# Optimization experiments

Measured on AMD Instinct MI355X. Metric: run time of the kernel, lower is better.

The kernel has to match this reference:

```python
import jax, jax.numpy as jnp
import numpy as np

B, L, C, H, W = 1, 16, 16, 128, 256  # L = T_chunk = K_chunk (single chunk, causal)
DECAY = 0.1  # decay_val


def setup_inputs() -> dict:
    key = jax.random.key(0)
    k1, k2 = jax.random.split(key)
    img = jax.random.normal(k1, (B, L, C, H, W), jnp.float32)
    # flows in normalized [-1,1] grid units; keep displacements modest
    cum_flow = jax.random.normal(k2, (B, L, 2, H, W), jnp.float32) * 0.1
    t = jnp.arange(L)
    mask = (t[:, None] >= t[None, :]).astype(jnp.float32)          # causal [T,K]
    decay_dist = jnp.abs(t[:, None] - t[None, :]).astype(jnp.float32)  # [T,K]
    return {"img": img, "cum_flow": cum_flow, "mask": mask, "decay_dist": decay_dist}


def _bilinear_sample(img, gx, gy):
    # img: [B,K,C,H,W]; gx, gy: [B,K,H,W] in normalized [-1,1] coords.
    # x wraps around (periodic), y clamps -- matching the kernel's index handling.
    ix = (gx + 1.0) * (W * 0.5) - 0.5
    iy = (gy + 1.0) * (H * 0.5) - 0.5
    x0 = jnp.floor(ix)
    y0 = jnp.floor(iy)
    wx = ix - x0  # fractional weights
    wy = iy - y0
    x0i = x0.astype(jnp.int32)
    y0i = y0.astype(jnp.int32)
    x0r = jnp.mod(x0i, W)
    x1r = jnpp = jnp.mod(x0i + 1, W)
    y0c = jnp.clip(y0i, 0, H - 1)
    y1c = jnp.clip(y0i + 1, 0, H - 1)

    K = img.shape[1]
    imgf = img.reshape(B, K, C, H * W)

    def gather(yy, xx):
        idx = (yy * W + xx).reshape(B, K, 1, H * W)  # broadcast over C
        return jnp.take_along_axis(imgf, idx, axis=-1).reshape(B, K, C, H, W)

    va = gather(y0c, x0r)  # (y0, x0)
    vb = gather(y1c, x0r)  # (y1, x0)
    vc = gather(y0c, x1r)  # (y0, x1)
    vd = gather(y1c, x1r)  # (y1, x1)
    wx_ = wx[:, :, None]   # [B,K,1,H,W]
    wy_ = wy[:, :, None]
    return (va * (1.0 - wx_) * (1.0 - wy_) + vb * (1.0 - wx_) * wy_
            + vc * wx_ * (1.0 - wy_) + vd * wx_ * wy_)


def reference(img, cum_flow, mask, decay_dist):
    # base grid (align_corners=False style pixel centers)
    base_x = (jnp.arange(W, dtype=jnp.float32) * (2.0 / W) - 1.0 + 1.0 / W)[None, None, :]  # [1,1,W]
    base_y = (jnp.arange(H, dtype=jnp.float32) * (2.0 / H) - 1.0 + 1.0 / H)[None, :, None]  # [1,H,1]

    weights = mask * jnp.exp(-DECAY * decay_dist)  # [T,K] decay-weighted causal mask
    fx = cum_flow[:, :, 0]  # [B,L,H,W]
    fy = cum_flow[:, :, 1]

    def step(carry, inp):
        ft_x, ft_y, w_row = inp  # ft_*: [B,H,W]; w_row: [K]
        gx = base_x[None] + (ft_x[:, None] - fx)  # [B,K,H,W]
        gy = base_y[None] + (ft_y[:, None] - fy)
        gx = jnp.mod(gx + 1.0, 2.0) - 1.0          # wrap x into [-1,1)
        sampled = _bilinear_sample(img, gx, gy)    # [B,K,C,H,W]
        out_t = jnp.einsum('k,bkchw->bchw', w_row, sampled)
        return carry, out_t

    xs = (jnp.moveaxis(fx, 1, 0), jnp.moveaxis(fy, 1, 0), weights)  # over t
    _, outs = jax.lax.scan(step, 0.0, xs)          # [T,B,C,H,W]
    return jnp.moveaxis(outs, 0, 1)                # [B,T,C,H,W]
```

## Files before the change

### kernel.cpp

```cpp
#include <hip/hip_runtime.h>
#include <hip/hip_fp16.h>

constexpr int Lc = 16;
constexpr int Cc = 16;
constexpr int Hc = 128;
constexpr int Wc = 256;
constexpr float DECAYc = 0.1f;
constexpr int HWc = Hc * Wc;

__global__ __launch_bounds__(256) void transpose_cvt_f16(
    const float* __restrict__ img, __half* __restrict__ imgTh)
{
    const int tid = threadIdx.x;
    const int h2 = tid & 1;
    const int wq = tid >> 1;
    const int kf  = blockIdx.x >> 5;
    const int px0 = (blockIdx.x & 31) * 1024;
    const float* __restrict__ srcb =
        img + (size_t)kf * Cc * HWc + (size_t)(8 * h2) * HWc;
#pragma unroll
    for (int rr = 0; rr < 8; ++rr) {
        const int px = px0 + rr * 128 + wq;
        float v[8];
#pragma unroll
        for (int c = 0; c < 8; ++c) v[c] = srcb[c * HWc + px];
        __half2 h[4];
#pragma unroll
        for (int i = 0; i < 4; ++i)
            h[i] = __float22half2_rn(make_float2(v[2 * i], v[2 * i + 1]));
        *(uint4*)(imgTh + ((size_t)kf * HWc + px) * Cc + 8 * h2) = *(uint4*)h;
    }
}

template <int T0>
__device__ __forceinline__ void chunk8(
    int k, const __half* __restrict__ bkq,
    const float* sx1, const float* sy1, float fxk, float fyk,
    const float* et, float ek, float4* acc)
{
    uint2 ld [8][4];
    float wts[8][4];
    int  offs[8][4];

#pragma unroll
    for (int j = 0; j < 8; ++j) {
        const int t = T0 + j;
        if (t >= Lc) continue;
        if (t > k) {
            const float wkt = et[t] * ek;

            float a = sx1[t] - fxk;
            a -= 2.0f * floorf(a * 0.5f);
            const float X  = a * (Wc * 0.5f) + 255.5f;
            const float Xf = floorf(X);
            const float wx = X - Xf;
            const int xp  = (int)Xf;
            const int x0r = xp & (Wc - 1);
            const int x1r = (xp + 1) & (Wc - 1);

            const float iy = (sy1[t] - fyk) * (Hc * 0.5f) - 0.5f;
            const float Yf = floorf(iy);
            const float wy = iy - Yf;
            const int y0  = (int)Yf;
            const int y0c = min(max(y0, 0), Hc - 1);
            const int y1c = min(max(y0 + 1, 0), Hc - 1);

            const float wb = wkt * wy;
            const float wa = wkt - wb;
            const float omx = 1.0f - wx;
            wts[j][0] = wa * omx;
            wts[j][1] = wa * wx;
            wts[j][2] = wb * omx;
            wts[j][3] = wb * wx;

            const int r0 = y0c << 8, r1 = y1c << 8;
            offs[j][0] = r0 | x0r;
            offs[j][1] = r0 | x1r;
            offs[j][2] = r1 | x0r;
            offs[j][3] = r1 | x1r;
        }
    }
#pragma unroll
    for (int j = 0; j < 8; ++j) {
        const int t = T0 + j;
        if (t >= Lc) continue;
        if (t > k) {
#pragma unroll
            for (int n = 0; n < 4; ++n)
                ld[j][n] = *(const uint2*)(bkq + (size_t)offs[j][n] * Cc);
        }
    }
#pragma unroll
    for (int j = 0; j < 8; ++j) {
        const int t = T0 + j;
        if (t >= Lc) continue;
        if (t > k) {
#pragma unroll
            for (int n = 0; n < 4; ++n) {
                const __half2* hp = (const __half2*)&ld[j][n];
                const float a = wts[j][n];
                acc[t].x += a * __half2float(__low2half (hp[0]));
                acc[t].y += a * __half2float(__high2half(hp[0]));
                acc[t].z += a * __half2float(__low2half (hp[1]));
                acc[t].w += a * __half2float(__high2half(hp[1]));
            }
        }
    }
}

__global__ __launch_bounds__(256, 2) void gridsample_f16(
    const __half* __restrict__ imgTh,
    const float* __restrict__ cum_flow,
    const float* __restrict__ img,
    float* __restrict__ out)
{
    const int tid = threadIdx.x;
    const int q  = tid & 3;
    const int wq = tid >> 2;
    const int b = blockIdx.x;
    const int band = b & 7;
    const int sub  = b >> 3;
    const int h = band * 16 + (sub >> 2);
    const int w = (sub & 3) * 64 + wq;
    const int pix = h * Wc + w;

    const float base_x = w * (2.0f / Wc) - 1.0f + 1.0f / Wc;
    const float base_y = h * (2.0f / Hc) - 1.0f + 1.0f / Hc;

    float sx1[Lc], sy1[Lc], et[Lc];
#pragma unroll
    for (int t = 0; t < Lc; ++t) {
        sx1[t] = base_x + cum_flow[(t * 2 + 0) * HWc + pix] + 1.0f;
        sy1[t] = base_y + cum_flow[(t * 2 + 1) * HWc + pix] + 1.0f;
        et[t]  = __expf(-DECAYc * (float)t);
    }

    float4 acc[Lc];
#pragma unroll
    for (int t = 0; t < Lc; ++t) acc[t] = make_float4(0.f, 0.f, 0.f, 0.f);

    float ek = 1.0f;
    for (int k = 0; k < Lc - 1; ++k) {
        const float fxk = cum_flow[(k * 2 + 0) * HWc + pix];
        const float fyk = cum_flow[(k * 2 + 1) * HWc + pix];
        const __half* __restrict__ bkq =
            imgTh + (size_t)k * HWc * Cc + 4 * q;

        chunk8<1>(k, bkq, sx1, sy1, fxk, fyk, et, ek, acc);
        chunk8<9>(k, bkq, sx1, sy1, fxk, fyk, et, ek, acc);

        ek *= 1.1051709180756477f;
    }

#pragma unroll
    for (int t = 0; t < Lc; ++t) {
        const float* __restrict__ ip = img + ((size_t)t * Cc + 4 * q) * HWc + pix;
        float* __restrict__ op = out + ((size_t)t * Cc + 4 * q) * HWc + pix;
        op[0 * HWc] = acc[t].x + ip[0 * HWc];
        op[1 * HWc] = acc[t].y + ip[1 * HWc];
        op[2 * HWc] = acc[t].z + ip[2 * HWc];
        op[3 * HWc] = acc[t].w + ip[3 * HWc];
    }
}

__global__ __launch_bounds__(256) void gridsample_warp_acc(
    const float* __restrict__ img, const float* __restrict__ cum_flow,
    const float* __restrict__ mask, const float* __restrict__ decay,
    float* __restrict__ out)
{
    const int w = threadIdx.x, h = blockIdx.x, t = blockIdx.y;
    const int pix = h * Wc + w;
    const float base_x = w * (2.0f / Wc) - 1.0f + 1.0f / Wc;
    const float base_y = h * (2.0f / Hc) - 1.0f + 1.0f / Hc;
    const float fxt = cum_flow[(t * 2 + 0) * HWc + pix];
    const float fyt = cum_flow[(t * 2 + 1) * HWc + pix];
    float acc[Cc];
#pragma unroll
    for (int c = 0; c < Cc; ++c) acc[c] = 0.0f;
    for (int k = 0; k <= t; ++k) {
        const float wkt = mask[t * Lc + k] * __expf(-DECAYc * decay[t * Lc + k]);
        const float fxk = cum_flow[(k * 2 + 0) * HWc + pix];
        const float fyk = cum_flow[(k * 2 + 1) * HWc + pix];
        float gx = base_x + (fxt - fxk);
        const float gy = base_y + (fyt - fyk);
        float m = gx + 1.0f;
        m -= 2.0f * floorf(m * 0.5f);
        gx = m - 1.0f;
        const float ix = (gx + 1.0f) * (Wc * 0.5f) - 0.5f;
        const float iy = (gy + 1.0f) * (Hc * 0.5f) - 0.5f;
        const float x0f = floorf(ix), y0f = floorf(iy);
        const float wx = ix - x0f, wy = iy - y0f;
        const int x0 = (int)x0f, y0 = (int)y0f;
        const int x0r = x0 & (Wc - 1), x1r = (x0 + 1) & (Wc - 1);
        const int y0c = min(max(y0, 0), Hc - 1), y1c = min(max(y0 + 1, 0), Hc - 1);
        const float a00 = wkt * (1.0f - wx) * (1.0f - wy);
        const float a01 = wkt * (1.0f - wx) * wy;
        const float a10 = wkt * wx * (1.0f - wy);
        const float a11 = wkt * wx * wy;
        const int o00 = y0c * Wc + x0r, o01 = y1c * Wc + x0r;
        const int o10 = y0c * Wc + x1r, o11 = y1c * Wc + x1r;
        const float* __restrict__ ik = img + (size_t)k * Cc * HWc;
#pragma unroll
        for (int c = 0; c < Cc; ++c) {
            const float* __restrict__ p = ik + c * HWc;
            acc[c] += p[o00] * a00 + p[o01] * a01 + p[o10] * a10 + p[o11] * a11;
        }
    }
    float* __restrict__ op = out + (size_t)t * Cc * HWc + pix;
#pragma unroll
    for (int c = 0; c < Cc; ++c) op[c * HWc] = acc[c];
}

extern "C" void kernel_launch(void* const* d_in, const int* in_sizes, int n_in,
                              void* d_out, int out_size, void* d_ws, size_t ws_size,
                              hipStream_t stream) {
    const float* img      = (const float*)d_in[0];
    const float* cum_flow = (const float*)d_in[1];
    const float* mask     = (const float*)d_in[2];
    const float* decay    = (const float*)d_in[3];
    float* out = (float*)d_out;

    const size_t needed = (size_t)Lc * HWc * Cc * sizeof(__half);
    if (ws_size >= needed) {
        __half* imgTh = (__half*)d_ws;
        transpose_cvt_f16<<<dim3(512), 256, 0, stream>>>(img, imgTh);
        gridsample_f16<<<dim3(512), 256, 0, stream>>>(imgTh, cum_flow, img, out);
    } else {
        dim3 grid(Hc, Lc, 1);
        gridsample_warp_acc<<<grid, Wc, 0, stream>>>(img, cum_flow, mask, decay, out);
    }
}
```

Before: 153.6 us.

## Fuse fp16 transpose into gridsample kernel with atomic grid barrier

Merges the fp16 channel-last transpose kernel into the grid-sample kernel. Every block first converts its slice of the image, then all blocks wait at a global spin barrier built from an atomic counter before sampling. This removes one kernel launch and the gap between kernels, but adds a memset launch and a spin barrier that only works if all 512 blocks are resident at once. The barrier has a guard-count timeout, so if blocks are not co-resident it falls through and could read imgTh before it is written.

```diff
diff --git a/kernel.cpp b/kernel.cpp
--- a/kernel.cpp
+++ b/kernel.cpp
@@ -7,30 +7,7 @@
 constexpr int Wc = 256;
 constexpr float DECAYc = 0.1f;
 constexpr int HWc = Hc * Wc;
-
-__global__ __launch_bounds__(256) void transpose_cvt_f16(
-    const float* __restrict__ img, __half* __restrict__ imgTh)
-{
-    const int tid = threadIdx.x;
-    const int h2 = tid & 1;
-    const int wq = tid >> 1;
-    const int kf  = blockIdx.x >> 5;
-    const int px0 = (blockIdx.x & 31) * 1024;
-    const float* __restrict__ srcb =
-        img + (size_t)kf * Cc * HWc + (size_t)(8 * h2) * HWc;
-#pragma unroll
-    for (int rr = 0; rr < 8; ++rr) {
-        const int px = px0 + rr * 128 + wq;
-        float v[8];
-#pragma unroll
-        for (int c = 0; c < 8; ++c) v[c] = srcb[c * HWc + px];
-        __half2 h[4];
-#pragma unroll
-        for (int i = 0; i < 4; ++i)
-            h[i] = __float22half2_rn(make_float2(v[2 * i], v[2 * i + 1]));
-        *(uint4*)(imgTh + ((size_t)kf * HWc + px) * Cc + 8 * h2) = *(uint4*)h;
-    }
-}
+constexpr unsigned NBLK = 512;
 
 template <int T0>
 __device__ __forceinline__ void chunk8(
@@ -108,16 +85,51 @@
     }
 }
 
-__global__ __launch_bounds__(256, 2) void gridsample_f16(
-    const __half* __restrict__ imgTh,
+__global__ __launch_bounds__(256, 2) void gridsample_fused2(
+    const float* __restrict__ img,
     const float* __restrict__ cum_flow,
-    const float* __restrict__ img,
+    __half* __restrict__ imgTh,
+    unsigned int* __restrict__ done,
     float* __restrict__ out)
 {
     const int tid = threadIdx.x;
+    const int b = blockIdx.x;
+
+    {
+        const int h2 = tid & 1;
+        const int wqa = tid >> 1;
+        const int kf  = b >> 5;
+        const int px0 = (b & 31) * 1024;
+        const float* __restrict__ srcb =
+            img + (size_t)kf * Cc * HWc + (size_t)(8 * h2) * HWc;
+#pragma unroll
+        for (int rr = 0; rr < 8; ++rr) {
+            const int px = px0 + rr * 128 + wqa;
+            float v[8];
+#pragma unroll
+            for (int c = 0; c < 8; ++c) v[c] = srcb[c * HWc + px];
+            __half2 hh[4];
+#pragma unroll
+            for (int i = 0; i < 4; ++i)
+                hh[i] = __float22half2_rn(make_float2(v[2 * i], v[2 * i + 1]));
+            *(uint4*)(imgTh + ((size_t)kf * HWc + px) * Cc + 8 * h2) = *(uint4*)hh;
+        }
+    }
+    __syncthreads();
+    if (tid == 0) {
+        __hip_atomic_fetch_add(done, 1u, __ATOMIC_RELEASE, __HIP_MEMORY_SCOPE_AGENT);
+        int guard = 0;
+        while (__hip_atomic_load(done, __ATOMIC_RELAXED, __HIP_MEMORY_SCOPE_AGENT)
+               < NBLK) {
+            __builtin_amdgcn_s_sleep(8);
+            if (++guard > (1 << 20)) break;
+        }
+    }
+    __syncthreads();
+    __builtin_amdgcn_fence(__ATOMIC_ACQUIRE, "agent");
+
     const int q  = tid & 3;
     const int wq = tid >> 2;
-    const int b = blockIdx.x;
     const int band = b & 7;
     const int sub  = b >> 3;
     const int h = band * 16 + (sub >> 2);
@@ -143,8 +155,7 @@
     for (int k = 0; k < Lc - 1; ++k) {
         const float fxk = cum_flow[(k * 2 + 0) * HWc + pix];
         const float fyk = cum_flow[(k * 2 + 1) * HWc + pix];
-        const __half* __restrict__ bkq =
-            imgTh + (size_t)k * HWc * Cc + 4 * q;
+        const __half* __restrict__ bkq = imgTh + (size_t)k * HWc * Cc + 4 * q;
 
         chunk8<1>(k, bkq, sx1, sy1, fxk, fyk, et, ek, acc);
         chunk8<9>(k, bkq, sx1, sy1, fxk, fyk, et, ek, acc);
@@ -220,11 +231,14 @@
     const float* decay    = (const float*)d_in[3];
     float* out = (float*)d_out;
 
-    const size_t needed = (size_t)Lc * HWc * Cc * sizeof(__half);
+    const size_t imgTh_bytes = (size_t)Lc * HWc * Cc * sizeof(__half);
+    const size_t needed = imgTh_bytes + 256;
     if (ws_size >= needed) {
         __half* imgTh = (__half*)d_ws;
-        transpose_cvt_f16<<<dim3(512), 256, 0, stream>>>(img, imgTh);
-        gridsample_f16<<<dim3(512), 256, 0, stream>>>(imgTh, cum_flow, img, out);
+        unsigned int* done = (unsigned int*)((char*)d_ws + imgTh_bytes);
+        hipMemsetAsync(done, 0, sizeof(unsigned int), stream);
+        gridsample_fused2<<<dim3(NBLK), 256, 0, stream>>>(
+            img, cum_flow, imgTh, done, out);
     } else {
         dim3 grid(Hc, Lc, 1);
         gridsample_warp_acc<<<grid, Wc, 0, stream>>>(img, cum_flow, mask, decay, out);
```

New measurement: 214.1 us. +39.4%, slower.

## Split output timesteps by parity across blocks to double parallelism

Applied to the files above, without the earlier changes.

Each block now handles only the even or the odd output timesteps for its pixels, so the grid grows from 512 to 1024 blocks and per-thread accumulator and register state is halved. Launch bounds are raised to allow 4 blocks per CU, aiming for more occupancy and better latency hiding on the gather loads. In exchange, per-k flow loads and the index and weight setup are repeated across the two parity blocks, and the causal work is split unevenly between the even and odd blocks.

```diff
diff --git a/kernel.cpp b/kernel.cpp
--- a/kernel.cpp
+++ b/kernel.cpp
@@ -32,24 +32,24 @@
     }
 }
 
-template <int T0>
-__device__ __forceinline__ void chunk8(
-    int k, const __half* __restrict__ bkq,
+template <int I0>
+__device__ __forceinline__ void chunk4p(
+    int k, int p, const __half* __restrict__ bkq,
     const float* sx1, const float* sy1, float fxk, float fyk,
-    const float* et, float ek, float4* acc)
-{
-    uint2 ld [8][4];
-    float wts[8][4];
-    int  offs[8][4];
-
-#pragma unroll
-    for (int j = 0; j < 8; ++j) {
-        const int t = T0 + j;
-        if (t >= Lc) continue;
+    const float* e2, float epk, float4* acc)
+{
+    uint2 ld [4][4];
+    float wts[4][4];
+    int  offs[4][4];
+
+#pragma unroll
+    for (int j = 0; j < 4; ++j) {
+        const int i = I0 + j;
+        const int t = 2 * i + p;
         if (t > k) {
-            const float wkt = et[t] * ek;
-
-            float a = sx1[t] - fxk;
+            const float wkt = e2[i] * epk;
+
+            float a = sx1[i] - fxk;
             a -= 2.0f * floorf(a * 0.5f);
             const float X  = a * (Wc * 0.5f) + 255.5f;
             const float Xf = floorf(X);
@@ -58,7 +58,7 @@
             const int x0r = xp & (Wc - 1);
             const int x1r = (xp + 1) & (Wc - 1);
 
-            const float iy = (sy1[t] - fyk) * (Hc * 0.5f) - 0.5f;
+            const float iy = (sy1[i] - fyk) * (Hc * 0.5f) - 0.5f;
             const float Yf = floorf(iy);
             const float wy = iy - Yf;
             const int y0  = (int)Yf;
@@ -81,9 +81,8 @@
         }
     }
 #pragma unroll
-    for (int j = 0; j < 8; ++j) {
-        const int t = T0 + j;
-        if (t >= Lc) continue;
+    for (int j = 0; j < 4; ++j) {
+        const int t = 2 * (I0 + j) + p;
         if (t > k) {
 #pragma unroll
             for (int n = 0; n < 4; ++n)
@@ -91,24 +90,24 @@
         }
     }
 #pragma unroll
-    for (int j = 0; j < 8; ++j) {
-        const int t = T0 + j;
-        if (t >= Lc) continue;
+    for (int j = 0; j < 4; ++j) {
+        const int i = I0 + j;
+        const int t = 2 * i + p;
         if (t > k) {
 #pragma unroll
             for (int n = 0; n < 4; ++n) {
                 const __half2* hp = (const __half2*)&ld[j][n];
                 const float a = wts[j][n];
-                acc[t].x += a * __half2float(__low2half (hp[0]));
-                acc[t].y += a * __half2float(__high2half(hp[0]));
-                acc[t].z += a * __half2float(__low2half (hp[1]));
-                acc[t].w += a * __half2float(__high2half(hp[1]));
+                acc[i].x += a * __half2float(__low2half (hp[0]));
+                acc[i].y += a * __half2float(__high2half(hp[0]));
+                acc[i].z += a * __half2float(__low2half (hp[1]));
+                acc[i].w += a * __half2float(__high2half(hp[1]));
             }
         }
     }
 }
 
-__global__ __launch_bounds__(256, 2) void gridsample_f16(
+__global__ __launch_bounds__(256, 4) void gridsample_f16_par(
     const __half* __restrict__ imgTh,
     const float* __restrict__ cum_flow,
     const float* __restrict__ img,
@@ -119,7 +118,8 @@
     const int wq = tid >> 2;
     const int b = blockIdx.x;
     const int band = b & 7;
-    const int sub  = b >> 3;
+    const int p    = (b >> 3) & 1;
+    const int sub  = b >> 4;
     const int h = band * 16 + (sub >> 2);
     const int w = (sub & 3) * 64 + wq;
     const int pix = h * Wc + w;
@@ -127,39 +127,41 @@
     const float base_x = w * (2.0f / Wc) - 1.0f + 1.0f / Wc;
     const float base_y = h * (2.0f / Hc) - 1.0f + 1.0f / Hc;
 
-    float sx1[Lc], sy1[Lc], et[Lc];
-#pragma unroll
-    for (int t = 0; t < Lc; ++t) {
-        sx1[t] = base_x + cum_flow[(t * 2 + 0) * HWc + pix] + 1.0f;
-        sy1[t] = base_y + cum_flow[(t * 2 + 1) * HWc + pix] + 1.0f;
-        et[t]  = __expf(-DECAYc * (float)t);
-    }
-
-    float4 acc[Lc];
-#pragma unroll
-    for (int t = 0; t < Lc; ++t) acc[t] = make_float4(0.f, 0.f, 0.f, 0.f);
-
-    float ek = 1.0f;
-    for (int k = 0; k < Lc - 1; ++k) {
+    float sx1[8], sy1[8], e2[8];
+#pragma unroll
+    for (int i = 0; i < 8; ++i) {
+        const int t = 2 * i + p;
+        sx1[i] = base_x + cum_flow[(t * 2 + 0) * HWc + pix] + 1.0f;
+        sy1[i] = base_y + cum_flow[(t * 2 + 1) * HWc + pix] + 1.0f;
+        e2[i]  = __expf(-2.0f * DECAYc * (float)i);
+    }
+
+    float4 acc[8];
+#pragma unroll
+    for (int i = 0; i < 8; ++i) acc[i] = make_float4(0.f, 0.f, 0.f, 0.f);
+
+    float epk = p ? 0.9048374180359595f : 1.0f;
+    const int kmax = 13 + p;
+    for (int k = 0; k <= kmax; ++k) {
         const float fxk = cum_flow[(k * 2 + 0) * HWc + pix];
         const float fyk = cum_flow[(k * 2 + 1) * HWc + pix];
-        const __half* __restrict__ bkq =
-            imgTh + (size_t)k * HWc * Cc + 4 * q;
-
-        chunk8<1>(k, bkq, sx1, sy1, fxk, fyk, et, ek, acc);
-        chunk8<9>(k, bkq, sx1, sy1, fxk, fyk, et, ek, acc);
-
-        ek *= 1.1051709180756477f;
-    }
-
-#pragma unroll
-    for (int t = 0; t < Lc; ++t) {
+        const __half* __restrict__ bkq = imgTh + (size_t)k * HWc * Cc + 4 * q;
+
+        chunk4p<0>(k, p, bkq, sx1, sy1, fxk, fyk, e2, epk, acc);
+        chunk4p<4>(k, p, bkq, sx1, sy1, fxk, fyk, e2, epk, acc);
+
+        epk *= 1.1051709180756477f;
+    }
+
+#pragma unroll
+    for (int i = 0; i < 8; ++i) {
+        const int t = 2 * i + p;
         const float* __restrict__ ip = img + ((size_t)t * Cc + 4 * q) * HWc + pix;
         float* __restrict__ op = out + ((size_t)t * Cc + 4 * q) * HWc + pix;
-        op[0 * HWc] = acc[t].x + ip[0 * HWc];
-        op[1 * HWc] = acc[t].y + ip[1 * HWc];
-        op[2 * HWc] = acc[t].z + ip[2 * HWc];
-        op[3 * HWc] = acc[t].w + ip[3 * HWc];
+        op[0 * HWc] = acc[i].x + ip[0 * HWc];
+        op[1 * HWc] = acc[i].y + ip[1 * HWc];
+        op[2 * HWc] = acc[i].z + ip[2 * HWc];
+        op[3 * HWc] = acc[i].w + ip[3 * HWc];
     }
 }
 
@@ -224,7 +226,8 @@
     if (ws_size >= needed) {
         __half* imgTh = (__half*)d_ws;
         transpose_cvt_f16<<<dim3(512), 256, 0, stream>>>(img, imgTh);
-        gridsample_f16<<<dim3(512), 256, 0, stream>>>(imgTh, cum_flow, img, out);
+        gridsample_f16_par<<<dim3(1024), 256, 0, stream>>>(
+            imgTh, cum_flow, img, out);
     } else {
         dim3 grid(Hc, Lc, 1);
         gridsample_warp_acc<<<grid, Wc, 0, stream>>>(img, cum_flow, mask, decay, out);
```

Result: no change. 151.5 us (-1.3%).
